# Performance work log

Measured on AMD Instinct MI355X. Metric: run time of the kernel, lower is better.

## Reference

```python
import jax, jax.numpy as jnp
import numpy as np

NODES = 16384                       # power of two -> all heap levels complete
DEPTH = (NODES - 1).bit_length() + 1  # 15 heap steps, linears k = 0..14
IN_F = 64
OUT_F = 64
MINHEAP = 0
BATCH = 32


def setup_inputs() -> dict:
    key = jax.random.key(0)
    k1, k2, k3 = jax.random.split(key, 3)
    x = jax.random.normal(k1, (BATCH, NODES, IN_F), dtype=jnp.float32)
    # stacked per-heap-step Linear params, torch layout W: [out, in]
    W = jax.random.normal(k2, (DEPTH - MINHEAP, OUT_F, IN_F), dtype=jnp.float32) * 0.05
    b = jax.random.normal(k3, (DEPTH - MINHEAP, OUT_F), dtype=jnp.float32) * 0.05
    return {"x": x, "W": W, "b": b}


def reference(x, W, b):
    # HeapLinear forward. Heap layout: level l occupies nodes [2^(l-1), 2^l)
    # (root = node 0, level(j) = bit_length(j)). The original double loop over
    # (input level l, linear k) with repeat_interleave(2^k) is equivalent to:
    #   output[j] = sum_{k=minheap}^{depth-1, level(j)>=k} linears[k](input[j >> k])
    # for power-of-two `nodes` (every out block satisfies out_node1 <= nodes).
    nodes = x.shape[-2]
    depth = (nodes - 1).bit_length() + 1
    j = np.arange(nodes)
    levels = np.array([int(v).bit_length() for v in j])  # static, trace-time
    out = jnp.zeros(x.shape[:-1] + (W.shape[1],), dtype=x.dtype)
    for k in range(MINHEAP, depth):
        n_anc = max(nodes >> k, 1)  # only nodes 0..n_anc-1 serve as distance-k ancestors
        # small per-level Linear applied to ancestor slice: [..., n_anc, out]
        t = jnp.einsum('...ni,oi->...no', x[..., :n_anc, :], W[k - MINHEAP]) + b[k - MINHEAP]
        anc = j >> k                      # distance-k ancestor of each node
        mask = levels >= k                # nodes shallower than k have no such ancestor
        out = out + jnp.where(mask[:, None], t[..., anc, :], jnp.zeros((), x.dtype))
    return out
```

## Files before the change

### kernel.cpp

```cpp
#include <hip/hip_runtime.h>

#define NODES 16384
#define NF 64
#define NBLK 128
#define TROW 72
#define BATCH 32

#define WS_WBF_OFF   0ull
#define WS_WT_OFF    122880ull
#define WS_BPRE_OFF  368640ull
#define WS_FAR_OFF   372480ull
#define WS_NEEDED    1421056ull

typedef __attribute__((ext_vector_type(8))) short short8;
typedef __attribute__((ext_vector_type(4))) short shortx4;
typedef __attribute__((ext_vector_type(4))) float floatx4;

__device__ __forceinline__ short f2bf(float f) {
    unsigned u = __float_as_uint(f);
    u += 0x7fffu + ((u >> 16) & 1u);
    return (short)(u >> 16);
}
__device__ __forceinline__ float bf2f(short s) {
    return __uint_as_float(((unsigned)(unsigned short)s) << 16);
}
__device__ __forceinline__ short8 cvt8(floatx4 a, floatx4 c) {
    short8 r;
    r[0]=f2bf(a[0]); r[1]=f2bf(a[1]); r[2]=f2bf(a[2]); r[3]=f2bf(a[3]);
    r[4]=f2bf(c[0]); r[5]=f2bf(c[1]); r[6]=f2bf(c[2]); r[7]=f2bf(c[3]);
    return r;
}

__global__ __launch_bounds__(256)
void heaplin_prep1(const float* __restrict__ W, const float* __restrict__ bias,
                   short* __restrict__ wbf, float* __restrict__ wt,
                   float* __restrict__ bpre)
{
    const int blk = blockIdx.x;
    const int tid = threadIdx.x;
    if (blk < 30) {
        int e = blk * 2048 + tid * 8;
        floatx4 a = *(const floatx4*)(W + e);
        floatx4 c = *(const floatx4*)(W + e + 4);
        *(short8*)(wbf + e) = cvt8(a, c);
    } else if (blk == 30) {
        if (tid < 64) {
            float run = 0.f;
            for (int k = 0; k < 15; ++k) { run += bias[k * 64 + tid]; bpre[k * 64 + tid] = run; }
        }
    } else {
        int k = blk - 31;
        #pragma unroll
        for (int it = 0; it < 16; ++it) {
            int idx = tid + it * 256;
            int o = idx >> 6, i = idx & 63;
            wt[k * 4096 + i * 64 + o] = W[k * 4096 + idx];
        }
    }
}

__global__ __launch_bounds__(256)
void heaplin_prep2(const float* __restrict__ x, const float* __restrict__ wt,
                   const float* __restrict__ bpre, float* __restrict__ far)
{
    __shared__ float xl[64 * 64];
    __shared__ float Zl[127 * 64];
    const int tid = threadIdx.x;
    const int b   = blockIdx.x;
    const float* xb = x + (size_t)b * NODES * NF;

    #pragma unroll
    for (int i = 0; i < 4; ++i) {
        int job = tid + i * 256;
        *(floatx4*)(xl + job * 4) = *(const floatx4*)(xb + job * 4);
    }
    __syncthreads();

    const int wave = tid >> 6, lane = tid & 63;
    const int o4 = lane & 15, j = lane >> 4;
    for (int r = wave; r < 127; r += 4) {
        int t, a;
        if (r < 64)       { t = 1; a = r; }
        else if (r < 96)  { t = 2; a = r - 64; }
        else if (r < 112) { t = 3; a = r - 96; }
        else if (r < 120) { t = 4; a = r - 112; }
        else if (r < 124) { t = 5; a = r - 120; }
        else if (r < 126) { t = 6; a = r - 124; }
        else              { t = 7; a = 0; }
        const float* wtk = wt + (7 + t) * 4096;
        floatx4 acc = {0.f, 0.f, 0.f, 0.f};
        #pragma unroll
        for (int i16 = 0; i16 < 16; ++i16) {
            int i = j + i16 * 4;
            floatx4 w4 = *(const floatx4*)(wtk + i * 64 + o4 * 4);
            float xs = xl[a * 64 + i];
            acc[0] += w4[0]*xs; acc[1] += w4[1]*xs; acc[2] += w4[2]*xs; acc[3] += w4[3]*xs;
        }
        #pragma unroll
        for (int c = 0; c < 4; ++c) {
            acc[c] += __shfl_xor(acc[c], 16, 64);
            acc[c] += __shfl_xor(acc[c], 32, 64);
        }
        if (j == 0) *(floatx4*)(Zl + r * 64 + o4 * 4) = acc;
    }
    __syncthreads();

    for (int it = 0; it < 32; ++it) {
        int job = tid + it * 256;
        if (job < 127 * 64) {
            int m = 1 + (job >> 6), o = job & 63;
            int bl = 32 - __clz(m);
            float s = bpre[(7 + bl) * 64 + o];
            #pragma unroll
            for (int t = 1; t <= 7; ++t)
                if (t <= bl) s += Zl[(128 - (128 >> (t - 1)) + (m >> t)) * 64 + o];
            far[((size_t)b * 128 + m) * 64 + o] = s;
        }
    }
}

__global__ __launch_bounds__(256, 2)
void heaplin_main(const float* __restrict__ x, const short* __restrict__ wbf,
                  const float* __restrict__ far, const float* __restrict__ bpre,
                  float* __restrict__ out)
{
    __shared__ short tbuf[128 * TROW];

    const int tid  = threadIdx.x;
    const int lane = tid & 63;
    const int wave = tid >> 6;
    const int lr = lane & 15;
    const int lq = lane >> 4;
    const int nblk = blockIdx.x;
    const int b    = blockIdx.y;
    const float* xb = x + (size_t)b * NODES * NF;
    float* ob = out + (size_t)b * NODES * NF;
    const floatx4 zero4 = {0.f, 0.f, 0.f, 0.f};

    if (nblk == 0) {
        floatx4 accE[8];
        #pragma unroll
        for (int t8 = 0; t8 < 8; ++t8) accE[t8] = zero4;

        for (int k = 0; k < 8; ++k) {
            __syncthreads();
            #pragma unroll
            for (int i = 0; i < 8; ++i) {
                int job = tid + i * 256;
                int r = job >> 4, c4 = job & 15;
                bool valid = (k == 0) || (r >= (1 << (k - 1)));
                floatx4 vv = zero4;
                if (valid) vv = *(const floatx4*)(xb + (r >> k) * NF + c4 * 4);
                shortx4 s4;
                s4[0]=f2bf(vv[0]); s4[1]=f2bf(vv[1]); s4[2]=f2bf(vv[2]); s4[3]=f2bf(vv[3]);
                *(shortx4*)(tbuf + r * TROW + c4 * 4) = s4;
            }
            __syncthreads();
            #pragma unroll
            for (int t8 = 0; t8 < 8; ++t8) {
                int mt = 2 * wave + (t8 & 1);
                int nt = t8 >> 1;
                int arow = mt * 16 + lr;
                const short* wp = wbf + k * 4096 + (nt * 16 + lr) * 64 + lq * 8;
                short8 b0 = *(const short8*)wp;
                short8 b1 = *(const short8*)(wp + 32);
                short8 a0 = *(const short8*)(tbuf + arow * TROW + lq * 8);
                short8 a1 = *(const short8*)(tbuf + arow * TROW + 32 + lq * 8);
                accE[t8] = __builtin_amdgcn_mfma_f32_16x16x32_bf16(b0, a0, accE[t8], 0, 0, 0);
                accE[t8] = __builtin_amdgcn_mfma_f32_16x16x32_bf16(b1, a1, accE[t8], 0, 0, 0);
            }
        }
        #pragma unroll
        for (int t8 = 0; t8 < 8; ++t8) {
            int mt = 2 * wave + (t8 & 1);
            int nt = t8 >> 1;
            int j  = mt * 16 + lr;
            int c4 = nt * 16 + lq * 4;
            int lvl = (j == 0) ? 0 : (32 - __clz(j));
            floatx4 bp = *(const floatx4*)(bpre + lvl * 64 + c4);
            floatx4 v;
            #pragma unroll
            for (int rg = 0; rg < 4; ++rg) v[rg] = accE[t8][rg] + bp[rg];
            *(floatx4*)(ob + (size_t)j * NF + c4) = v;
        }
        return;
    }

    const int n0 = nblk * NBLK;

    const float* apA = xb + (size_t)(n0 + 2 * wave * 16 + lr) * NF + lq * 8;
    const float* apB = apA + 16 * NF;
    floatx4 fA0 = *(const floatx4*)apA,        fA1 = *(const floatx4*)(apA + 4);
    floatx4 fA2 = *(const floatx4*)(apA + 32), fA3 = *(const floatx4*)(apA + 36);
    floatx4 fB0 = *(const floatx4*)apB,        fB1 = *(const floatx4*)(apB + 4);
    floatx4 fB2 = *(const floatx4*)(apB + 32), fB3 = *(const floatx4*)(apB + 36);

    const int mD  = tid >> 2;
    const int c0D = (tid & 3) * 16;
    floatx4 fvv[4];
    {
        const float* fv = far + ((size_t)b * 128 + nblk) * 64 + c0D;
        #pragma unroll
        for (int i = 0; i < 4; ++i) fvv[i] = *(const floatx4*)(fv + i * 4);
    }

    #pragma unroll
    for (int g = 0; g < 3; ++g) {
        const int idx = wave + g * 4;
        const bool gvalid = (idx < 11);
        const int idxc = gvalid ? idx : 0;
        int k, mt;
        if (idxc < 4)       { k = 1; mt = idxc; }
        else if (idxc < 6)  { k = 2; mt = idxc - 4; }
        else if (idxc == 6) { k = 3; mt = 0; }
        else                { k = idxc - 3; mt = 0; }
        const int anc = n0 >> k;
        const int rowb = (anc & ~15) + mt * 16;
        const float* ap = xb + (size_t)(rowb + lr) * NF + lq * 8;
        floatx4 f0 = *(const floatx4*)ap,        f1 = *(const floatx4*)(ap + 4);
        floatx4 f2 = *(const floatx4*)(ap + 32), f3 = *(const floatx4*)(ap + 36);
        short8 a0 = cvt8(f0, f1), a1 = cvt8(f2, f3);
        const int tb  = 128 - (256 >> k);
        const int cnt = 128 >> k;
        const int off = anc & 15;
        int row; bool rvalid;
        if (k <= 3) { row = tb + mt * 16 + lr; rvalid = true; }
        else        { row = tb + lr - off;     rvalid = (lr >= off) && (lr < off + cnt); }
        #pragma unroll
        for (int nt = 0; nt < 4; ++nt) {
            const short* wp = wbf + k * 4096 + (nt * 16 + lr) * 64 + lq * 8;
            short8 b0 = *(const short8*)wp;
            short8 b1 = *(const short8*)(wp + 32);
            floatx4 acc = zero4;
            acc = __builtin_amdgcn_mfma_f32_16x16x32_bf16(b0, a0, acc, 0, 0, 0);
            acc = __builtin_amdgcn_mfma_f32_16x16x32_bf16(b1, a1, acc, 0, 0, 0);
            if (gvalid && rvalid) {
                shortx4 s4;
                s4[0]=f2bf(acc[0]); s4[1]=f2bf(acc[1]); s4[2]=f2bf(acc[2]); s4[3]=f2bf(acc[3]);
                *(shortx4*)(tbuf + row * TROW + nt * 16 + lq * 4) = s4;
            }
        }
    }

    floatx4 accE[8];
    {
        short8 aA0 = cvt8(fA0, fA1), aA1 = cvt8(fA2, fA3);
        short8 aB0 = cvt8(fB0, fB1), aB1 = cvt8(fB2, fB3);
        #pragma unroll
        for (int nt = 0; nt < 4; ++nt) {
            const short* wp = wbf + (nt * 16 + lr) * 64 + lq * 8;
            short8 b0 = *(const short8*)wp;
            short8 b1 = *(const short8*)(wp + 32);
            floatx4 accA = zero4, accB = zero4;
            accA = __builtin_amdgcn_mfma_f32_16x16x32_bf16(b0, aA0, accA, 0, 0, 0);
            accA = __builtin_amdgcn_mfma_f32_16x16x32_bf16(b1, aA1, accA, 0, 0, 0);
            accB = __builtin_amdgcn_mfma_f32_16x16x32_bf16(b0, aB0, accB, 0, 0, 0);
            accB = __builtin_amdgcn_mfma_f32_16x16x32_bf16(b1, aB1, accB, 0, 0, 0);
            accE[2 * nt + 0] = accA;
            accE[2 * nt + 1] = accB;
        }
    }
    __syncthreads();

    {
        const short* tb0 = tbuf + mD                * TROW + c0D;
        const short* tb1 = tbuf + (64  + (mD >> 1)) * TROW + c0D;
        const short* tb2 = tbuf + (96  + (mD >> 2)) * TROW + c0D;
        const short* tb3 = tbuf + (112 + (mD >> 3)) * TROW + c0D;
        const short* tb4 = tbuf + (120 + (mD >> 4)) * TROW + c0D;
        const short* tb5 = tbuf + (124 + (mD >> 5)) * TROW + c0D;
        const short* tb6 = tbuf + 126               * TROW + c0D;
        short8 r0a = *(const short8*)tb0, r0b = *(const short8*)(tb0 + 8);
        short8 r1a = *(const short8*)tb1, r1b = *(const short8*)(tb1 + 8);
        short8 r2a = *(const short8*)tb2, r2b = *(const short8*)(tb2 + 8);
        short8 r3a = *(const short8*)tb3, r3b = *(const short8*)(tb3 + 8);
        short8 r4a = *(const short8*)tb4, r4b = *(const short8*)(tb4 + 8);
        short8 r5a = *(const short8*)tb5, r5b = *(const short8*)(tb5 + 8);
        short8 r6a = *(const short8*)tb6, r6b = *(const short8*)(tb6 + 8);
        float e[16];
        #pragma unroll
        for (int i = 0; i < 8; ++i) {
            e[i]     = bf2f(r0a[i]) + bf2f(r1a[i]) + bf2f(r2a[i]) + bf2f(r3a[i])
                     + bf2f(r4a[i]) + bf2f(r5a[i]) + bf2f(r6a[i]) + fvv[i >> 2][i & 3];
            e[i + 8] = bf2f(r0b[i]) + bf2f(r1b[i]) + bf2f(r2b[i]) + bf2f(r3b[i])
                     + bf2f(r4b[i]) + bf2f(r5b[i]) + bf2f(r6b[i]) + fvv[(i + 8) >> 2][i & 3];
        }
        __syncthreads();
        short8 wlo, whi;
        #pragma unroll
        for (int i = 0; i < 8; ++i) { wlo[i] = f2bf(e[i]); whi[i] = f2bf(e[i + 8]); }
        *(short8*)(tbuf + mD * TROW + c0D)     = wlo;
        *(short8*)(tbuf + mD * TROW + c0D + 8) = whi;
    }
    __syncthreads();

    #pragma unroll
    for (int t8 = 0; t8 < 8; ++t8) {
        int mt = 2 * wave + (t8 & 1);
        int nt = t8 >> 1;
        int j  = mt * 16 + lr;
        int c4 = nt * 16 + lq * 4;
        shortx4 u = *(const shortx4*)(tbuf + (mt * 8 + (lr >> 1)) * TROW + c4);
        floatx4 v;
        #pragma unroll
        for (int rg = 0; rg < 4; ++rg) v[rg] = accE[t8][rg] + bf2f(u[rg]);
        *(floatx4*)(ob + (size_t)(n0 + j) * NF + c4) = v;
    }
}

#define SROW 72
#define SROWS 270
__global__ __launch_bounds__(256, 4)
void heaplin_fallback(const float* __restrict__ x, const float* __restrict__ W,
                      const float* __restrict__ bias, float* __restrict__ out)
{
    __shared__ short stage[SROWS * SROW];
    __shared__ float farpart[4 * 64];
    short* tbuf = stage;
    float* cumB = (float*)(stage + 128 * SROW);

    const int tid  = threadIdx.x;
    const int lane = tid & 63;
    const int wave = tid >> 6;
    const int lr = lane & 15;
    const int lq = lane >> 4;
    const int nblk = blockIdx.x;
    const int b    = blockIdx.y;
    const float* xb = x + (size_t)b * NODES * NF;
    float* ob = out + (size_t)b * NODES * NF;
    const floatx4 zero4 = {0.f, 0.f, 0.f, 0.f};

    if (nblk == 0) {
        if (tid < 64) {
            float run = 0.f;
            for (int k = 0; k < 15; ++k) { run += bias[k * 64 + tid]; cumB[k * 64 + tid] = run; }
        }
        floatx4 accE[8];
        #pragma unroll
        for (int t8 = 0; t8 < 8; ++t8) accE[t8] = zero4;
        for (int k = 0; k < 8; ++k) {
            __syncthreads();
            #pragma unroll
            for (int i = 0; i < 8; ++i) {
                int job = tid + i * 256;
                int r = job >> 4, c4 = job & 15;
                bool valid = (k == 0) || (r >= (1 << (k - 1)));
                floatx4 vv = zero4;
                if (valid) vv = *(const floatx4*)(xb + (r >> k) * NF + c4 * 4);
                shortx4 s4;
                s4[0]=f2bf(vv[0]); s4[1]=f2bf(vv[1]); s4[2]=f2bf(vv[2]); s4[3]=f2bf(vv[3]);
                *(shortx4*)(stage + r * SROW + c4 * 4) = s4;
            }
            __syncthreads();
            #pragma unroll
            for (int t8 = 0; t8 < 8; ++t8) {
                int mt = 2 * wave + (t8 & 1);
                int nt = t8 >> 1;
                int arow = mt * 16 + lr;
                const float* wr = W + k * 4096 + (nt * 16 + lr) * 64 + lq * 8;
                floatx4 wa = *(const floatx4*)wr, wb2 = *(const floatx4*)(wr + 4);
                short8 b0 = cvt8(wa, wb2);
                floatx4 wc = *(const floatx4*)(wr + 32), wd = *(const floatx4*)(wr + 36);
                short8 b1 = cvt8(wc, wd);
                short8 a0 = *(const short8*)(stage + arow * SROW + lq * 8);
                short8 a1 = *(const short8*)(stage + arow * SROW + 32 + lq * 8);
                accE[t8] = __builtin_amdgcn_mfma_f32_16x16x32_bf16(a0, b0, accE[t8], 0, 0, 0);
                accE[t8] = __builtin_amdgcn_mfma_f32_16x16x32_bf16(a1, b1, accE[t8], 0, 0, 0);
            }
        }
        #pragma unroll
        for (int t8 = 0; t8 < 8; ++t8) {
            int mt = 2 * wave + (t8 & 1);
            int nt = t8 >> 1;
            int c = nt * 16 + lr;
            #pragma unroll
            for (int rg = 0; rg < 4; ++rg) {
                int j = mt * 16 + lq * 4 + rg;
                int lvl = (j == 0) ? 0 : (32 - __clz(j));
                ob[(size_t)j * NF + c] = accE[t8][rg] + cumB[lvl * 64 + c];
            }
        }
        return;
    }

    const int n0 = nblk * NBLK;
    const int L  = 32 - __clz(n0);
    floatx4 v[16];
    #pragma unroll
    for (int i = 0; i < 16; ++i) {
        int job = tid + i * 256;
        int r = job >> 4, c4 = job & 15;
        int node;
        if (r < 128)        node = n0 + r;
        else if (r >= 254)  node = n0 >> 7;
        else { int k = __clz(255 - r) - 24; node = (n0 >> k) + r - (256 - (256 >> k)); }
        v[i] = *(const floatx4*)(xb + (size_t)node * NF + c4 * 4);
    }
    #pragma unroll
    for (int i = 0; i < 16; ++i) {
        int job = tid + i * 256;
        int r = job >> 4, c4 = job & 15;
        shortx4 s4;
        s4[0]=f2bf(v[i][0]); s4[1]=f2bf(v[i][1]); s4[2]=f2bf(v[i][2]); s4[3]=f2bf(v[i][3]);
        *(shortx4*)(stage + r * SROW + c4 * 4) = s4;
    }
    __syncthreads();
    floatx4 accE[8];
    #pragma unroll
    for (int t8 = 0; t8 < 8; ++t8) {
        int mt = 2 * wave + (t8 & 1);
        int nt = t8 >> 1;
        int arow = mt * 16 + lr;
        const float* wr = W + (nt * 16 + lr) * 64 + lq * 8;
        floatx4 wa = *(const floatx4*)wr, wb2 = *(const floatx4*)(wr + 4);
        short8 b0 = cvt8(wa, wb2);
        floatx4 wc = *(const floatx4*)(wr + 32), wd = *(const floatx4*)(wr + 36);
        short8 b1 = cvt8(wc, wd);
        short8 a0 = *(const short8*)(stage + arow * SROW + lq * 8);
        short8 a1 = *(const short8*)(stage + arow * SROW + 32 + lq * 8);
        floatx4 acc = zero4;
        acc = __builtin_amdgcn_mfma_f32_16x16x32_bf16(a0, b0, acc, 0, 0, 0);
        acc = __builtin_amdgcn_mfma_f32_16x16x32_bf16(a1, b1, acc, 0, 0, 0);
        accE[t8] = acc;
    }
    {
        float p = 0.f;
        const int q = wave, o = lane;
        for (int k = 8; k <= L; ++k) {
            const float* xa = xb + (size_t)(n0 >> k) * NF + q * 16;
            const float* wr = W + k * 4096 + o * 64 + q * 16;
            #pragma unroll
            for (int i = 0; i < 4; ++i) {
                floatx4 wv = *(const floatx4*)(wr + i * 4);
                floatx4 xv = *(const floatx4*)(xa + i * 4);
                p += wv[0]*xv[0] + wv[1]*xv[1] + wv[2]*xv[2] + wv[3]*xv[3];
            }
        }
        if (q == 0) for (int k = 0; k <= L; ++k) p += bias[k * 64 + o];
        farpart[q * 64 + o] = p;
    }
    __syncthreads();
    for (int jj = 0; jj < 11; ++jj) {
        int job = wave + jj * 4;
        int idx = job % 11;
        int nt  = job / 11;
        int k, mt;
        if (idx < 4)      { k = 1; mt = idx; }
        else if (idx < 6) { k = 2; mt = idx - 4; }
        else if (idx < 7) { k = 3; mt = 0; }
        else              { k = idx - 3; mt = 0; }
        int sbase = 256 - (256 >> k);
        int arow = sbase + mt * 16 + lr;
        const float* wr = W + k * 4096 + (nt * 16 + lr) * 64 + lq * 8;
        floatx4 wa = *(const floatx4*)wr, wb2 = *(const floatx4*)(wr + 4);
        short8 b0 = cvt8(wa, wb2);
        floatx4 wc = *(const floatx4*)(wr + 32), wd = *(const floatx4*)(wr + 36);
        short8 b1 = cvt8(wc, wd);
        short8 a0 = *(const short8*)(stage + arow * SROW + lq * 8);
        short8 a1 = *(const short8*)(stage + arow * SROW + 32 + lq * 8);
        floatx4 acc = zero4;
        acc = __builtin_amdgcn_mfma_f32_16x16x32_bf16(a0, b0, acc, 0, 0, 0);
        acc = __builtin_amdgcn_mfma_f32_16x16x32_bf16(a1, b1, acc, 0, 0, 0);
        int tb = 128 - (256 >> k);
        int nvalid = 128 >> k;
        #pragma unroll
        for (int rg = 0; rg < 4; ++rg) {
            int m = mt * 16 + lq * 4 + rg;
            if (m < nvalid) tbuf[(tb + m) * TROW + nt * 16 + lr] = f2bf(acc[rg]);
        }
    }
    __syncthreads();
    {
        int m  = tid >> 2;
        int c0 = (tid & 3) * 16;
        float e[16];
        #pragma unroll
        for (int i = 0; i < 16; ++i) {
            int c = c0 + i;
            e[i] = bf2f(tbuf[ m               * TROW + c])
                 + bf2f(tbuf[(64  + (m >> 1)) * TROW + c])
                 + bf2f(tbuf[(96  + (m >> 2)) * TROW + c])
                 + bf2f(tbuf[(112 + (m >> 3)) * TROW + c])
                 + bf2f(tbuf[(120 + (m >> 4)) * TROW + c])
                 + bf2f(tbuf[(124 + (m >> 5)) * TROW + c])
                 + bf2f(tbuf[126              * TROW + c])
                 + farpart[c] + farpart[64 + c] + farpart[128 + c] + farpart[192 + c];
        }
        #pragma unroll
        for (int i = 0; i < 16; ++i) tbuf[m * TROW + c0 + i] = f2bf(e[i]);
    }
    __syncthreads();
    #pragma unroll
    for (int t8 = 0; t8 < 8; ++t8) {
        int mt = 2 * wave + (t8 & 1);
        int nt = t8 >> 1;
        int c = nt * 16 + lr;
        #pragma unroll
        for (int rg = 0; rg < 4; ++rg) {
            int j = mt * 16 + lq * 4 + rg;
            float val = accE[t8][rg] + bf2f(tbuf[(j >> 1) * TROW + c]);
            ob[(size_t)(n0 + j) * NF + c] = val;
        }
    }
}

extern "C" void kernel_launch(void* const* d_in, const int* in_sizes, int n_in,
                              void* d_out, int out_size, void* d_ws, size_t ws_size,
                              hipStream_t stream) {
    const float* x  = (const float*)d_in[0];
    const float* W  = (const float*)d_in[1];
    const float* bs = (const float*)d_in[2];
    float* out = (float*)d_out;
    dim3 grid(NODES / NBLK, BATCH);
    if (ws_size >= WS_NEEDED) {
        short* wbf  = (short*)((char*)d_ws + WS_WBF_OFF);
        float* wt   = (float*)((char*)d_ws + WS_WT_OFF);
        float* bpre = (float*)((char*)d_ws + WS_BPRE_OFF);
        float* farb = (float*)((char*)d_ws + WS_FAR_OFF);
        heaplin_prep1<<<46, 256, 0, stream>>>(W, bs, wbf, wt, bpre);
        heaplin_prep2<<<32, 256, 0, stream>>>(x, wt, bpre, farb);
        heaplin_main<<<grid, 256, 0, stream>>>(x, wbf, farb, bpre, out);
    } else {
        heaplin_fallback<<<grid, 256, 0, stream>>>(x, W, bs, out);
    }
}
```

Measured before the change: 344.0 us.

## Stage x tiles through LDS with coalesced row loads before MFMA

The main kernel now loads all 19 needed 16-row x tiles (the block's own rows plus ancestor tiles) with fully coalesced row-contiguous loads, converts them to bf16 and stores them in a larger LDS staging buffer. Both the self MFMA and the ancestor MFMAs then read their A operands from LDS instead of doing strided per-lane global loads. The intent is better global coalescing and earlier issue of all loads. The launch bound is raised to 3 blocks/CU, and the reduction phase is restructured to cut live registers and drop one barrier. The cost is extra LDS traffic, a bigger shared footprint that may limit occupancy, and an added barrier.

```diff
diff --git a/kernel.cpp b/kernel.cpp
--- a/kernel.cpp
+++ b/kernel.cpp
@@ -5,6 +5,7 @@
 #define NBLK 128
 #define TROW 72
 #define BATCH 32
+#define NTILES 19
 
 #define WS_WBF_OFF   0ull
 #define WS_WT_OFF    122880ull
@@ -29,6 +30,15 @@
     r[0]=f2bf(a[0]); r[1]=f2bf(a[1]); r[2]=f2bf(a[2]); r[3]=f2bf(a[3]);
     r[4]=f2bf(c[0]); r[5]=f2bf(c[1]); r[6]=f2bf(c[2]); r[7]=f2bf(c[3]);
     return r;
+}
+
+__device__ __forceinline__ int tile_base(int t, int n0) {
+    if (t < 8)   return n0 + t * 16;
+    if (t < 12)  return (n0 >> 1) + (t - 8) * 16;
+    if (t < 14)  return (n0 >> 2) + (t - 12) * 16;
+    if (t == 14) return (n0 >> 3);
+    int k = t - 11;
+    return (n0 >> k) & ~15;
 }
 
 __global__ __launch_bounds__(256)
@@ -119,12 +129,13 @@
     }
 }
 
-__global__ __launch_bounds__(256, 2)
+__global__ __launch_bounds__(256, 3)
 void heaplin_main(const float* __restrict__ x, const short* __restrict__ wbf,
                   const float* __restrict__ far, const float* __restrict__ bpre,
                   float* __restrict__ out)
 {
-    __shared__ short tbuf[128 * TROW];
+    __shared__ short stage[NTILES * 16 * TROW];
+    short* tbuf = stage;
 
     const int tid  = threadIdx.x;
     const int lane = tid & 63;
@@ -188,12 +199,15 @@
 
     const int n0 = nblk * NBLK;
 
-    const float* apA = xb + (size_t)(n0 + 2 * wave * 16 + lr) * NF + lq * 8;
-    const float* apB = apA + 16 * NF;
-    floatx4 fA0 = *(const floatx4*)apA,        fA1 = *(const floatx4*)(apA + 4);
-    floatx4 fA2 = *(const floatx4*)(apA + 32), fA3 = *(const floatx4*)(apA + 36);
-    floatx4 fB0 = *(const floatx4*)apB,        fB1 = *(const floatx4*)(apB + 4);
-    floatx4 fB2 = *(const floatx4*)(apB + 32), fB3 = *(const floatx4*)(apB + 36);
+    floatx4 sv[20];
+    #pragma unroll
+    for (int i = 0; i < 5; ++i) {
+        int t = wave * 5 + i; if (t > 18) t = 18;
+        const float* src = xb + (size_t)(tile_base(t, n0) + (lane >> 4)) * NF + (lane & 15) * 4;
+        #pragma unroll
+        for (int it = 0; it < 4; ++it)
+            sv[i * 4 + it] = *(const floatx4*)(src + it * 4 * NF);
+    }
 
     const int mD  = tid >> 2;
     const int c0D = (tid & 3) * 16;
@@ -205,21 +219,53 @@
     }
 
     #pragma unroll
+    for (int i = 0; i < 5; ++i) {
+        int t = wave * 5 + i; if (t > 18) t = 18;
+        #pragma unroll
+        for (int it = 0; it < 4; ++it) {
+            floatx4 v = sv[i * 4 + it];
+            shortx4 s4;
+            s4[0]=f2bf(v[0]); s4[1]=f2bf(v[1]); s4[2]=f2bf(v[2]); s4[3]=f2bf(v[3]);
+            *(shortx4*)(stage + (t * 16 + it * 4 + (lane >> 4)) * TROW + (lane & 15) * 4) = s4;
+        }
+    }
+    __syncthreads();
+
+    floatx4 accE[8];
+    {
+        const short* pa = stage + ((2 * wave)     * 16 + lr) * TROW + lq * 8;
+        const short* pb = stage + ((2 * wave + 1) * 16 + lr) * TROW + lq * 8;
+        short8 aA0 = *(const short8*)pa, aA1 = *(const short8*)(pa + 32);
+        short8 aB0 = *(const short8*)pb, aB1 = *(const short8*)(pb + 32);
+        #pragma unroll
+        for (int nt = 0; nt < 4; ++nt) {
+            const short* wp = wbf + (nt * 16 + lr) * 64 + lq * 8;
+            short8 b0 = *(const short8*)wp;
+            short8 b1 = *(const short8*)(wp + 32);
+            floatx4 accA = zero4, accB = zero4;
+            accA = __builtin_amdgcn_mfma_f32_16x16x32_bf16(b0, aA0, accA, 0, 0, 0);
+            accA = __builtin_amdgcn_mfma_f32_16x16x32_bf16(b1, aA1, accA, 0, 0, 0);
+            accB = __builtin_amdgcn_mfma_f32_16x16x32_bf16(b0, aB0, accB, 0, 0, 0);
+            accB = __builtin_amdgcn_mfma_f32_16x16x32_bf16(b1, aB1, accB, 0, 0, 0);
+            accE[2 * nt + 0] = accA;
+            accE[2 * nt + 1] = accB;
+        }
+    }
+    __syncthreads();
+
+    #pragma unroll
     for (int g = 0; g < 3; ++g) {
         const int idx = wave + g * 4;
         const bool gvalid = (idx < 11);
         const int idxc = gvalid ? idx : 0;
-        int k, mt;
-        if (idxc < 4)       { k = 1; mt = idxc; }
-        else if (idxc < 6)  { k = 2; mt = idxc - 4; }
-        else if (idxc == 6) { k = 3; mt = 0; }
-        else                { k = idxc - 3; mt = 0; }
+        int k, mt, tIdx;
+        if (idxc < 4)       { k = 1; mt = idxc;     tIdx = 8 + mt; }
+        else if (idxc < 6)  { k = 2; mt = idxc - 4; tIdx = 12 + mt; }
+        else if (idxc == 6) { k = 3; mt = 0;        tIdx = 14; }
+        else                { k = idxc - 3; mt = 0; tIdx = 11 + k; }
         const int anc = n0 >> k;
-        const int rowb = (anc & ~15) + mt * 16;
-        const float* ap = xb + (size_t)(rowb + lr) * NF + lq * 8;
-        floatx4 f0 = *(const floatx4*)ap,        f1 = *(const floatx4*)(ap + 4);
-        floatx4 f2 = *(const floatx4*)(ap + 32), f3 = *(const floatx4*)(ap + 36);
-        short8 a0 = cvt8(f0, f1), a1 = cvt8(f2, f3);
+        const short* pa = stage + (tIdx * 16 + lr) * TROW + lq * 8;
+        short8 a0 = *(const short8*)pa, a1 = *(const short8*)(pa + 32);
         const int tb  = 128 - (256 >> k);
         const int cnt = 128 >> k;
         const int off = anc & 15;
@@ -241,56 +287,26 @@
             }
         }
     }
-
-    floatx4 accE[8];
-    {
-        short8 aA0 = cvt8(fA0, fA1), aA1 = cvt8(fA2, fA3);
-        short8 aB0 = cvt8(fB0, fB1), aB1 = cvt8(fB2, fB3);
-        #pragma unroll
-        for (int nt = 0; nt < 4; ++nt) {
-            const short* wp = wbf + (nt * 16 + lr) * 64 + lq * 8;
-            short8 b0 = *(const short8*)wp;
-            short8 b1 = *(const short8*)(wp + 32);
-            floatx4 accA = zero4, accB = zero4;
-            accA = __builtin_amdgcn_mfma_f32_16x16x32_bf16(b0, aA0, accA, 0, 0, 0);
-            accA = __builtin_amdgcn_mfma_f32_16x16x32_bf16(b1, aA1, accA, 0, 0, 0);
-            accB = __builtin_amdgcn_mfma_f32_16x16x32_bf16(b0, aB0, accB, 0, 0, 0);
-            accB = __builtin_amdgcn_mfma_f32_16x16x32_bf16(b1, aB1, accB, 0, 0, 0);
-            accE[2 * nt + 0] = accA;
-            accE[2 * nt + 1] = accB;
-        }
-    }
-    __syncthreads();
-
-    {
-        const short* tb0 = tbuf + mD                * TROW + c0D;
-        const short* tb1 = tbuf + (64  + (mD >> 1)) * TROW + c0D;
-        const short* tb2 = tbuf + (96  + (mD >> 2)) * TROW + c0D;
-        const short* tb3 = tbuf + (112 + (mD >> 3)) * TROW + c0D;
-        const short* tb4 = tbuf + (120 + (mD >> 4)) * TROW + c0D;
-        const short* tb5 = tbuf + (124 + (mD >> 5)) * TROW + c0D;
-        const short* tb6 = tbuf + 126               * TROW + c0D;
-        short8 r0a = *(const short8*)tb0, r0b = *(const short8*)(tb0 + 8);
-        short8 r1a = *(const short8*)tb1, r1b = *(const short8*)(tb1 + 8);
-        short8 r2a = *(const short8*)tb2, r2b = *(const short8*)(tb2 + 8);
-        short8 r3a = *(const short8*)tb3, r3b = *(const short8*)(tb3 + 8);
-        short8 r4a = *(const short8*)tb4, r4b = *(const short8*)(tb4 + 8);
-        short8 r5a = *(const short8*)tb5, r5b = *(const short8*)(tb5 + 8);
-        short8 r6a = *(const short8*)tb6, r6b = *(const short8*)(tb6 + 8);
-        float e[16];
-        #pragma unroll
-        for (int i = 0; i < 8; ++i) {
-            e[i]     = bf2f(r0a[i]) + bf2f(r1a[i]) + bf2f(r2a[i]) + bf2f(r3a[i])
-                     + bf2f(r4a[i]) + bf2f(r5a[i]) + bf2f(r6a[i]) + fvv[i >> 2][i & 3];
-            e[i + 8] = bf2f(r0b[i]) + bf2f(r1b[i]) + bf2f(r2b[i]) + bf2f(r3b[i])
-                     + bf2f(r4b[i]) + bf2f(r5b[i]) + bf2f(r6b[i]) + fvv[(i + 8) >> 2][i & 3];
-        }
-        __syncthreads();
-        short8 wlo, whi;
-        #pragma unroll
-        for (int i = 0; i < 8; ++i) { wlo[i] = f2bf(e[i]); whi[i] = f2bf(e[i + 8]); }
-        *(short8*)(tbuf + mD * TROW + c0D)     = wlo;
-        *(short8*)(tbuf + mD * TROW + c0D + 8) = whi;
+    __syncthreads();
+
+    #pragma unroll
+    for (int q = 0; q < 4; ++q) {
+        const int cq = c0D + q * 4;
+        shortx4 r0 = *(const shortx4*)(tbuf +  mD               * TROW + cq);
+        shortx4 r1 = *(const shortx4*)(tbuf + (64  + (mD >> 1)) * TROW + cq);
+        shortx4 r2 = *(const shortx4*)(tbuf + (96  + (mD >> 2)) * TROW + cq);
+        shortx4 r3 = *(const shortx4*)(tbuf + (112 + (mD >> 3)) * TROW + cq);
+        shortx4 r4 = *(const shortx4*)(tbuf + (120 + (mD >> 4)) * TROW + cq);
+        shortx4 r5 = *(const shortx4*)(tbuf + (124 + (mD >> 5)) * TROW + cq);
+        shortx4 r6 = *(const shortx4*)(tbuf + 126               * TROW + cq);
+        shortx4 w;
+        #pragma unroll
+        for (int i = 0; i < 4; ++i) {
+            float e = bf2f(r0[i]) + bf2f(r1[i]) + bf2f(r2[i]) + bf2f(r3[i])
+                    + bf2f(r4[i]) + bf2f(r5[i]) + bf2f(r6[i]) + fvv[q][i];
+            w[i] = f2bf(e);
+        }
+        *(shortx4*)(tbuf + mD * TROW + cq) = w;
     }
     __syncthreads();
 
@@ -477,17 +493,17 @@
         #pragma unroll
         for (int i = 0; i < 16; ++i) {
             int c = c0 + i;
-            e[i] = bf2f(tbuf[ m               * TROW + c])
-                 + bf2f(tbuf[(64  + (m >> 1)) * TROW + c])
-                 + bf2f(tbuf[(96  + (m >> 2)) * TROW + c])
-                 + bf2f(tbuf[(112 + (m >> 3)) * TROW + c])
-                 + bf2f(tbuf[(120 + (m >> 4)) * TROW + c])
-                 + bf2f(tbuf[(124 + (m >> 5)) * TROW + c])
-                 + bf2f(tbuf[126              * TROW + c])
+            e[i] = bf2f(tbuf[ m               * SROW + c])
+                 + bf2f(tbuf[(64  + (m >> 1)) * SROW + c])
+                 + bf2f(tbuf[(96  + (m >> 2)) * SROW + c])
+                 + bf2f(tbuf[(112 + (m >> 3)) * SROW + c])
+                 + bf2f(tbuf[(120 + (m >> 4)) * SROW + c])
+                 + bf2f(tbuf[(124 + (m >> 5)) * SROW + c])
+                 + bf2f(tbuf[126              * SROW + c])
                  + farpart[c] + farpart[64 + c] + farpart[128 + c] + farpart[192 + c];
         }
         #pragma unroll
-        for (int i = 0; i < 16; ++i) tbuf[m * TROW + c0 + i] = f2bf(e[i]);
+        for (int i = 0; i < 16; ++i) tbuf[m * SROW + c0 + i] = f2bf(e[i]);
     }
     __syncthreads();
     #pragma unroll
@@ -498,7 +514,7 @@
         #pragma unroll
         for (int rg = 0; rg < 4; ++rg) {
             int j = mt * 16 + lq * 4 + rg;
-            float val = accE[t8][rg] + bf2f(tbuf[(j >> 1) * TROW + c]);
+            float val = accE[t8][rg] + bf2f(tbuf[(j >> 1) * SROW + c]);
             ob[(size_t)(n0 + j) * NF + c] = val;
         }
     }
```

Result: faster. 327.9 us (-4.7%).
